# Kernel optimization log

Hardware: AMD Instinct MI355X
Metric: run time of the kernel (lower is better)

## Reference

```python
import jax, jax.numpy as jnp
import numpy as np

VOCAB = 100000
EMB = 300      # embd_dim
S = 40         # sequence_length
B = 8192
C = 210        # out_channels
KH = 3         # kernel_height
DH = 35        # dense_hidden
NC = 35        # n_classes
KPOOL = S - KH + 1          # 38: MaxPool2d kernel height
NBLK = C // KPOOL           # 5: pool blocks over the channel dim (last 20 chans dropped)


def setup_inputs() -> dict:
    key = jax.random.key(0)
    ks = jax.random.split(key, 9)
    return {
        "x": jax.random.randint(ks[0], (B, S), 0, VOCAB, dtype=jnp.int64 if jax.config.jax_enable_x64 else jnp.int32),
        "pos_": jax.random.randint(ks[1], (B, 2), 0, S, dtype=jnp.int64 if jax.config.jax_enable_x64 else jnp.int32),
        "w2v": jax.random.normal(ks[2], (VOCAB, EMB), jnp.float32) * 0.1,
        "conv_w": jax.random.normal(ks[3], (KH, EMB, C), jnp.float32) * 0.02,   # WIO layout
        "conv_b": jax.random.normal(ks[4], (C,), jnp.float32) * 0.02,
        "dense_w": jax.random.normal(ks[5], (3 * S, DH), jnp.float32) * 0.05,
        "dense_b": jax.random.normal(ks[6], (DH,), jnp.float32) * 0.05,
        "out_w": jax.random.normal(ks[7], (DH, NC), jnp.float32) * 0.05,
        "out_b": jax.random.normal(ks[8], (NC,), jnp.float32) * 0.05,
    }


def reference(x, pos_, w2v, conv_w, conv_b, dense_w, dense_b, out_w, out_b):
    # Embedding lookup: [B, S, EMB]
    emb = w2v[x]
    # Conv2d(1, C, (KH, EMB), padding=(1, 0)) == 1D conv over seq with full-width kernel
    c = jax.lax.conv_general_dilated(
        emb, conv_w, window_strides=(1,), padding=[(1, 1)],
        dimension_numbers=("NWC", "WIO", "NWC"))  # [B, S, C]
    c = jax.nn.relu(c + conv_b)
    c = jnp.transpose(c, (0, 2, 1))  # [B, C, S], matches conv.squeeze(3)

    # ep1/ep2 normalization (faithful to the python loop)
    ep1 = jnp.minimum(pos_[:, 0], pos_[:, 1])
    ep2 = jnp.maximum(pos_[:, 0], pos_[:, 1])
    shift = (ep1 == 0).astype(ep1.dtype)
    ep1 = ep1 + shift
    ep2 = ep2 + shift

    pos = jnp.arange(S)
    m1 = (pos[None, :] < ep1[:, None]).astype(c.dtype)                                  # before e1
    m2 = ((pos[None, :] >= ep1[:, None]) & (pos[None, :] < ep2[:, None])).astype(c.dtype)  # between
    m3 = (pos[None, :] >= ep2[:, None]).astype(c.dtype)                                 # after e2

    def pool(m):
        # mask along seq, then MaxPool2d((38,1)) on a 3D tensor pools the CHANNEL dim
        y = c * m[:, None, :]                                  # [B, C, S]
        y = y[:, : NBLK * KPOOL, :].reshape(y.shape[0], NBLK, KPOOL, S)
        return y.max(axis=2)                                   # [B, NBLK, S]

    pooled = jnp.concatenate([pool(m1), pool(m2), pool(m3)], axis=2)  # [B, NBLK, 3S]
    pooled = pooled.reshape(-1, 3 * S)                                # [NBLK*B, 3S]
    h = pooled @ dense_w + dense_b
    return h @ out_w + out_b  # [NBLK*B, NC]
```

## Files before the change

### kernel.cpp

```cpp
#include <hip/hip_runtime.h>

typedef short bf16x8 __attribute__((ext_vector_type(8)));
typedef float f32x4 __attribute__((ext_vector_type(4)));
typedef unsigned short u16;
typedef u16 ushort8v __attribute__((ext_vector_type(8)));

#define VOCAB 100000
#define EMB 300
#define SEQ 40
#define BATCH 8192
#define COUT 210
#define NBLK 5
#define KPOOL 38
#define DH 35
#define NCLS 35
#define PCOL 320
#define KDIM 960
#define NUSE 192
#define BM 80
#define EROWS 84
#define ASTR 197
#define NGR 120

__device__ __forceinline__ u16 f2bf(float f) {
  unsigned u = __float_as_uint(f);
  unsigned r = 0x7FFFu + ((u >> 16) & 1u);
  return (u16)((u + r) >> 16);
}

__device__ __forceinline__ void gload_lds16(void* lds, const void* g) {
  __builtin_amdgcn_global_load_lds(
      (const __attribute__((address_space(1))) void*)g,
      (__attribute__((address_space(3))) void*)lds, 16, 0, 0);
}

__global__ __launch_bounds__(256) void k_prepW(const float* __restrict__ w2v,
                                               u16* __restrict__ W) {
  int id = blockIdx.x * 256 + threadIdx.x;
  if (id >= (VOCAB + 1) * 40) return;
  int v = id / 40, e8 = id - v * 40;
  int e = e8 * 8;
  float vals[8] = {0.f, 0.f, 0.f, 0.f, 0.f, 0.f, 0.f, 0.f};
  if (v < VOCAB) {
    const float* src = w2v + (size_t)v * EMB + e;
    if (e <= 292) {
      float4 f0 = *(const float4*)src;
      float4 f1 = *(const float4*)(src + 4);
      vals[0] = f0.x; vals[1] = f0.y; vals[2] = f0.z; vals[3] = f0.w;
      vals[4] = f1.x; vals[5] = f1.y; vals[6] = f1.z; vals[7] = f1.w;
    } else if (e == 296) {
      float4 f0 = *(const float4*)src;
      vals[0] = f0.x; vals[1] = f0.y; vals[2] = f0.z; vals[3] = f0.w;
    }
  }
  ushort8v o;
#pragma unroll
  for (int j = 0; j < 8; ++j) o[j] = f2bf(vals[j]);
  *(ushort8v*)(W + (size_t)v * PCOL + e) = o;
}

__global__ __launch_bounds__(256) void k_prepB(const float* __restrict__ convw,
                                               u16* __restrict__ Btn) {
  int id = blockIdx.x * 256 + threadIdx.x;
  if (id >= NGR * NUSE) return;
  int gg = id / NUSE, col = id - gg * NUSE;
  ushort8v o;
#pragma unroll
  for (int j = 0; j < 8; ++j) {
    int k = gg * 8 + j;
    int kh = (k >= 640) ? 2 : (k >= 320 ? 1 : 0);
    int e = k - kh * PCOL;
    float v = (e < EMB) ? convw[(kh * EMB + e) * COUT + col] : 0.f;
    o[j] = f2bf(v);
  }
  *(ushort8v*)(Btn + (size_t)id * 8) = o;
}

__global__ __launch_bounds__(256) void k_conv_gemm(const u16* __restrict__ Wb,
                                                   const u16* __restrict__ Btn,
                                                   const int* __restrict__ x,
                                                   const float* __restrict__ convb,
                                                   float* __restrict__ maxc) {
  __shared__ __align__(16) char smem[40 * EROWS * 16];
  float* act = (float*)smem;

  const int tid = threadIdx.x;
  const int lane = tid & 63;
  const int wc = tid >> 6;
  const int l15 = lane & 15, l4 = lane >> 4;
  const int b0 = blockIdx.x * 2;

#pragma unroll
  for (int ri = 0; ri < 13; ++ri) {
    const int d = ri * 256 + tid;
    const int g = d / EROWS, prow = d - g * EROWS;
    const int bb = prow / 42, sp = prow - bb * 42;
    const int tok = (sp == 0 || sp == 41) ? VOCAB : x[(b0 + bb) * SEQ + sp - 1];
    gload_lds16(smem + d * 16, Wb + (size_t)tok * PCOL + g * 8);
  }
  if (tid < 32) {
    const int d = 3328 + tid;
    const int g = d / EROWS, prow = d - g * EROWS;
    const int bb = prow / 42, sp = prow - bb * 42;
    const int tok = (sp == 0 || sp == 41) ? VOCAB : x[(b0 + bb) * SEQ + sp - 1];
    gload_lds16(smem + d * 16, Wb + (size_t)tok * PCOL + g * 8);
  }

  const int rA0 = l15;
  const int rA1 = 16 + l15;
  const int rA2 = 32 + l15 + ((l15 >= 8) ? 2 : 0);
  const int rA3 = 50 + l15;
  const int rA4 = 66 + l15;

  const u16* pbB = Btn + (size_t)((l4 * NUSE) + wc * 48 + l15) * 8;

  f32x4 acc[5][3];
  const f32x4 zero = {0.f, 0.f, 0.f, 0.f};
#pragma unroll
  for (int i = 0; i < 5; ++i)
#pragma unroll
    for (int j = 0; j < 3; ++j) acc[i][j] = zero;

  bf16x8 aR[2][5];
  bf16x8 bs[3][3];

#define LOADB(SI, T)                                                           \
  {                                                                            \
    const u16* p_ = pbB + (size_t)(T) * 6144;                                  \
    bs[SI][0] = *(const bf16x8*)(p_);                                          \
    bs[SI][1] = *(const bf16x8*)(p_ + 128);                                    \
    bs[SI][2] = *(const bf16x8*)(p_ + 256);                                    \
  }

#define LOADA(SL, T)                                                           \
  {                                                                            \
    const char* kb_ = smem + ((((T) % 10) * 4 + l4) * EROWS + (T) / 10) * 16;  \
    aR[SL][0] = *(const bf16x8*)(kb_ + rA0 * 16);                              \
    aR[SL][1] = *(const bf16x8*)(kb_ + rA1 * 16);                              \
    aR[SL][2] = *(const bf16x8*)(kb_ + rA2 * 16);                              \
    aR[SL][3] = *(const bf16x8*)(kb_ + rA3 * 16);                              \
    aR[SL][4] = *(const bf16x8*)(kb_ + rA4 * 16);                              \
  }

  LOADB(0, 0)
  LOADB(1, 1)
  __syncthreads();
  LOADA(0, 0)

#pragma unroll
  for (int t = 0; t < 30; ++t) {
    if (t + 1 < 30) { LOADA((t + 1) & 1, t + 1) }
    if (t + 2 < 30) { LOADB((t + 2) % 3, t + 2) }
    __builtin_amdgcn_s_setprio(1);
#pragma unroll
    for (int fn = 0; fn < 3; ++fn) {
      acc[0][fn] = __builtin_amdgcn_mfma_f32_16x16x32_bf16(aR[t & 1][0], bs[t % 3][fn], acc[0][fn], 0, 0, 0);
      acc[1][fn] = __builtin_amdgcn_mfma_f32_16x16x32_bf16(aR[t & 1][1], bs[t % 3][fn], acc[1][fn], 0, 0, 0);
      acc[2][fn] = __builtin_amdgcn_mfma_f32_16x16x32_bf16(aR[t & 1][2], bs[t % 3][fn], acc[2][fn], 0, 0, 0);
      acc[3][fn] = __builtin_amdgcn_mfma_f32_16x16x32_bf16(aR[t & 1][3], bs[t % 3][fn], acc[3][fn], 0, 0, 0);
      acc[4][fn] = __builtin_amdgcn_mfma_f32_16x16x32_bf16(aR[t & 1][4], bs[t % 3][fn], acc[4][fn], 0, 0, 0);
    }
    __builtin_amdgcn_s_setprio(0);
  }
#undef LOADA
#undef LOADB

  __syncthreads();

#pragma unroll
  for (int fm = 0; fm < 5; ++fm) {
#pragma unroll
    for (int fn = 0; fn < 3; ++fn) {
      const int col = wc * 48 + fn * 16 + l15;
      const float bias = convb[col];
#pragma unroll
      for (int rg = 0; rg < 4; ++rg) {
        const int rloc = l4 * 4 + rg;
        float vv = acc[fm][fn][rg] + bias;
        act[rloc * ASTR + col] = fmaxf(vv, 0.f);
      }
    }
    __syncthreads();
    if (tid < 80) {
      const int rl = tid / 5, gq = tid - rl * 5;
      const float* ap = act + rl * ASTR + gq * KPOOL;
      float mx = 0.f;
#pragma unroll
      for (int i = 0; i < KPOOL; ++i) mx = fmaxf(mx, ap[i]);
      const int mloc = fm * 16 + rl;
      const int bb = (mloc >= 40) ? 1 : 0;
      const int ss = mloc - 40 * bb;
      maxc[((b0 + bb) * NBLK + gq) * SEQ + ss] = mx;
    }
    __syncthreads();
  }
}

__global__ __launch_bounds__(256) void k_dense(const float* __restrict__ maxc,
                                               const int* __restrict__ pos,
                                               const float* __restrict__ dw,
                                               const float* __restrict__ db,
                                               const float* __restrict__ ow,
                                               const float* __restrict__ ob,
                                               float* __restrict__ out) {
  __shared__ float dwL[120 * 36];
  __shared__ float owL[35 * 36];
  __shared__ float hL[64 * 36];
  __shared__ float mxL[64 * 40];
  const int tid = threadIdx.x;
  const int r0 = blockIdx.x * 64;
  for (int i = tid; i < 120 * 35; i += 256) { int j = i / 35, d = i - j * 35; dwL[j * 36 + d] = dw[i]; }
  for (int i = tid; i < 35 * 35; i += 256)  { int j = i / 35, d = i - j * 35; owL[j * 36 + d] = ow[i]; }
  for (int i = tid; i < 64 * 40; i += 256)  mxL[i] = maxc[(size_t)r0 * 40 + i];
  __syncthreads();
  for (int t = tid; t < 64 * 35; t += 256) {
    const int row = t / 35, d = t - row * 35;
    const int rg = r0 + row;
    const int b = rg / NBLK;
    const int p0 = pos[b * 2], p1 = pos[b * 2 + 1];
    int e1 = min(p0, p1), e2 = max(p0, p1);
    if (e1 == 0) { e1 = 1; e2 += 1; }
    float a = db[d];
#pragma unroll
    for (int s = 0; s < SEQ; ++s) {
      const int k = (s >= e1) + (s >= e2);
      a += mxL[row * 40 + s] * dwL[(k * SEQ + s) * 36 + d];
    }
    hL[row * 36 + d] = a;
  }
  __syncthreads();
  for (int t = tid; t < 64 * 35; t += 256) {
    const int row = t / 35, c = t - row * 35;
    float a = ob[c];
#pragma unroll
    for (int d = 0; d < DH; ++d) a += hL[row * 36 + d] * owL[d * 36 + c];
    out[(size_t)(r0 + row) * NCLS + c] = a;
  }
}

extern "C" void kernel_launch(void* const* d_in, const int* in_sizes, int n_in,
                              void* d_out, int out_size, void* d_ws, size_t ws_size,
                              hipStream_t stream) {
  const int*   x     = (const int*)d_in[0];
  const int*   pos   = (const int*)d_in[1];
  const float* w2v   = (const float*)d_in[2];
  const float* convw = (const float*)d_in[3];
  const float* convb = (const float*)d_in[4];
  const float* dw    = (const float*)d_in[5];
  const float* db    = (const float*)d_in[6];
  const float* ow    = (const float*)d_in[7];
  const float* ob    = (const float*)d_in[8];
  float* out = (float*)d_out;

  char* ws = (char*)d_ws;
  u16* W    = (u16*)ws;
  u16* Btn  = (u16*)(ws + 64000640);
  float* maxc = (float*)(ws + 64000640 + 368640);

  k_prepW<<<15626, 256, 0, stream>>>(w2v, W);
  k_prepB<<<90, 256, 0, stream>>>(convw, Btn);
  k_conv_gemm<<<4096, 256, 0, stream>>>(W, Btn, x, convb, maxc);
  k_dense<<<640, 256, 0, stream>>>(maxc, pos, dw, db, ow, ob, out);
}
```

Before: 182.7 us.

## Split embedding LDS staging into two phases to shrink shared memory

The conv GEMM kernel now stages the gathered embedding rows into LDS in two phases: the first 28 of 40 k-groups, then the remaining 12 reusing the same buffer. LDS per block drops from 40 to 28 slots, which may let more blocks share a CU. In exchange it adds an extra barrier and a second gather-load phase that is not overlapped with MFMA work, so the second chunk's load latency is exposed.

```diff
diff --git a/kernel.cpp b/kernel.cpp
--- a/kernel.cpp
+++ b/kernel.cpp
@@ -15,10 +15,10 @@
 #define DH 35
 #define NCLS 35
 #define PCOL 320
-#define KDIM 960
 #define NUSE 192
 #define BM 80
 #define EROWS 84
+#define GSLOT 28
 #define ASTR 197
 #define NGR 120
 
@@ -81,7 +81,7 @@
                                                    const int* __restrict__ x,
                                                    const float* __restrict__ convb,
                                                    float* __restrict__ maxc) {
-  __shared__ __align__(16) char smem[40 * EROWS * 16];
+  __shared__ __align__(16) char smem[GSLOT * EROWS * 16];
   float* act = (float*)smem;
 
   const int tid = threadIdx.x;
@@ -89,22 +89,6 @@
   const int wc = tid >> 6;
   const int l15 = lane & 15, l4 = lane >> 4;
   const int b0 = blockIdx.x * 2;
-
-#pragma unroll
-  for (int ri = 0; ri < 13; ++ri) {
-    const int d = ri * 256 + tid;
-    const int g = d / EROWS, prow = d - g * EROWS;
-    const int bb = prow / 42, sp = prow - bb * 42;
-    const int tok = (sp == 0 || sp == 41) ? VOCAB : x[(b0 + bb) * SEQ + sp - 1];
-    gload_lds16(smem + d * 16, Wb + (size_t)tok * PCOL + g * 8);
-  }
-  if (tid < 32) {
-    const int d = 3328 + tid;
-    const int g = d / EROWS, prow = d - g * EROWS;
-    const int bb = prow / 42, sp = prow - bb * 42;
-    const int tok = (sp == 0 || sp == 41) ? VOCAB : x[(b0 + bb) * SEQ + sp - 1];
-    gload_lds16(smem + d * 16, Wb + (size_t)tok * PCOL + g * 8);
-  }
 
   const int rA0 = l15;
   const int rA1 = 16 + l15;
@@ -132,9 +116,9 @@
     bs[SI][2] = *(const bf16x8*)(p_ + 256);                                    \
   }
 
-#define LOADA(SL, T)                                                           \
+#define LOADA(SL, QD, KH)                                                      \
   {                                                                            \
-    const char* kb_ = smem + ((((T) % 10) * 4 + l4) * EROWS + (T) / 10) * 16;  \
+    const char* kb_ = smem + (((QD) * 4 + l4) * EROWS + (KH)) * 16;            \
     aR[SL][0] = *(const bf16x8*)(kb_ + rA0 * 16);                              \
     aR[SL][1] = *(const bf16x8*)(kb_ + rA1 * 16);                              \
     aR[SL][2] = *(const bf16x8*)(kb_ + rA2 * 16);                              \
@@ -142,28 +126,76 @@
     aR[SL][4] = *(const bf16x8*)(kb_ + rA4 * 16);                              \
   }
 
+#define MFMAS(SL, SB)                                                          \
+  __builtin_amdgcn_s_setprio(1);                                               \
+  _Pragma("unroll")                                                            \
+  for (int fn = 0; fn < 3; ++fn) {                                             \
+    acc[0][fn] = __builtin_amdgcn_mfma_f32_16x16x32_bf16(aR[SL][0], bs[SB][fn], acc[0][fn], 0, 0, 0); \
+    acc[1][fn] = __builtin_amdgcn_mfma_f32_16x16x32_bf16(aR[SL][1], bs[SB][fn], acc[1][fn], 0, 0, 0); \
+    acc[2][fn] = __builtin_amdgcn_mfma_f32_16x16x32_bf16(aR[SL][2], bs[SB][fn], acc[2][fn], 0, 0, 0); \
+    acc[3][fn] = __builtin_amdgcn_mfma_f32_16x16x32_bf16(aR[SL][3], bs[SB][fn], acc[3][fn], 0, 0, 0); \
+    acc[4][fn] = __builtin_amdgcn_mfma_f32_16x16x32_bf16(aR[SL][4], bs[SB][fn], acc[4][fn], 0, 0, 0); \
+  }                                                                            \
+  __builtin_amdgcn_s_setprio(0);
+
+#pragma unroll
+  for (int ri = 0; ri < 9; ++ri) {
+    const int d = ri * 256 + tid;
+    const int g = d / EROWS, prow = d - g * EROWS;
+    const int bb = prow / 42, sp = prow - bb * 42;
+    const int tok = (sp == 0 || sp == 41) ? VOCAB : x[(b0 + bb) * SEQ + sp - 1];
+    gload_lds16(smem + d * 16, Wb + (size_t)tok * PCOL + g * 8);
+  }
+  if (tid < 48) {
+    const int d = 2304 + tid;
+    const int g = d / EROWS, prow = d - g * EROWS;
+    const int bb = prow / 42, sp = prow - bb * 42;
+    const int tok = (sp == 0 || sp == 41) ? VOCAB : x[(b0 + bb) * SEQ + sp - 1];
+    gload_lds16(smem + d * 16, Wb + (size_t)tok * PCOL + g * 8);
+  }
   LOADB(0, 0)
   LOADB(1, 1)
   __syncthreads();
-  LOADA(0, 0)
-
-#pragma unroll
-  for (int t = 0; t < 30; ++t) {
-    if (t + 1 < 30) { LOADA((t + 1) & 1, t + 1) }
-    if (t + 2 < 30) { LOADB((t + 2) % 3, t + 2) }
-    __builtin_amdgcn_s_setprio(1);
-#pragma unroll
-    for (int fn = 0; fn < 3; ++fn) {
-      acc[0][fn] = __builtin_amdgcn_mfma_f32_16x16x32_bf16(aR[t & 1][0], bs[t % 3][fn], acc[0][fn], 0, 0, 0);
-      acc[1][fn] = __builtin_amdgcn_mfma_f32_16x16x32_bf16(aR[t & 1][1], bs[t % 3][fn], acc[1][fn], 0, 0, 0);
-      acc[2][fn] = __builtin_amdgcn_mfma_f32_16x16x32_bf16(aR[t & 1][2], bs[t % 3][fn], acc[2][fn], 0, 0, 0);
-      acc[3][fn] = __builtin_amdgcn_mfma_f32_16x16x32_bf16(aR[t & 1][3], bs[t % 3][fn], acc[3][fn], 0, 0, 0);
-      acc[4][fn] = __builtin_amdgcn_mfma_f32_16x16x32_bf16(aR[t & 1][4], bs[t % 3][fn], acc[4][fn], 0, 0, 0);
-    }
-    __builtin_amdgcn_s_setprio(0);
+
+  LOADA(0, 0, 0)
+#pragma unroll
+  for (int s = 0; s < 21; ++s) {
+    if (s + 1 < 21) { LOADA((s + 1) & 1, (s + 1) % 7, (s + 1) / 7) }
+    if (s + 2 < 21) { const int n = s + 2; LOADB(n % 3, (n / 7) * 10 + (n % 7)) }
+    MFMAS(s & 1, s % 3)
+  }
+
+  __syncthreads();
+
+#pragma unroll
+  for (int ri = 0; ri < 3; ++ri) {
+    const int d = ri * 256 + tid;
+    const int g = d / EROWS, prow = d - g * EROWS;
+    const int bb = prow / 42, sp = prow - bb * 42;
+    const int tok = (sp == 0 || sp == 41) ? VOCAB : x[(b0 + bb) * SEQ + sp - 1];
+    gload_lds16(smem + d * 16, Wb + (size_t)tok * PCOL + (GSLOT + g) * 8);
+  }
+  if (tid < 240) {
+    const int d = 768 + tid;
+    const int g = d / EROWS, prow = d - g * EROWS;
+    const int bb = prow / 42, sp = prow - bb * 42;
+    const int tok = (sp == 0 || sp == 41) ? VOCAB : x[(b0 + bb) * SEQ + sp - 1];
+    gload_lds16(smem + d * 16, Wb + (size_t)tok * PCOL + (GSLOT + g) * 8);
+  }
+  LOADB(0, 7)
+  LOADB(1, 8)
+  __syncthreads();
+
+  LOADA(0, 0, 0)
+#pragma unroll
+  for (int s = 0; s < 9; ++s) {
+    if (s + 1 < 9) { LOADA((s + 1) & 1, (s + 1) % 3, (s + 1) / 3) }
+    if (s + 2 < 9) { const int n = s + 2; LOADB(n % 3, (n / 3) * 10 + 7 + (n % 3)) }
+    MFMAS(s & 1, s % 3)
   }
 #undef LOADA
 #undef LOADB
+#undef MFMAS
 
   __syncthreads();
 
```

Result: slower. 199.1 us (+9.0%).
